# Performance work log

Hardware: AMD Instinct MI355X
Metric: run time of the kernel (lower is better)

## Reference

```python
import jax, jax.numpy as jnp
import numpy as np


def _gcn_conv(x, W, b, src, dst, n_nodes):
    # PyG GCNConv with add_self_loops=True, edge_weight=None (implicit ones),
    # symmetric normalization: D^{-1/2} A_hat D^{-1/2} (X W) + b
    xw = x @ W                                    # [N, H]
    loop = jnp.arange(n_nodes, dtype=src.dtype)
    src_f = jnp.concatenate([src, loop])          # [E+N]
    dst_f = jnp.concatenate([dst, loop])          # [E+N]
    w = jnp.ones(src_f.shape[0], dtype=x.dtype)
    deg = jax.ops.segment_sum(w, dst_f, num_segments=n_nodes)  # in-degree incl. self-loop
    dinv = jnp.where(deg > 0, jax.lax.rsqrt(deg), 0.0)
    norm = dinv[src_f] * dinv[dst_f]              # [E+N]
    msgs = norm[:, None] * xw[src_f]              # [E+N, H]
    out = jax.ops.segment_sum(msgs, dst_f, num_segments=n_nodes)
    return out + b


def setup_inputs() -> dict:
    key = jax.random.key(0)
    k1, k2, k3, k4 = jax.random.split(key, 4)
    N, E, D, H = 100000, 1600000, 256, 128
    x = jax.random.normal(k1, (N, D), dtype=jnp.float32)
    edge_index = jax.random.randint(k2, (2, E), 0, N, dtype=jnp.int64)
    # Glorot-scaled weights
    W1 = jax.random.normal(k3, (D, H), dtype=jnp.float32) * np.sqrt(2.0 / (D + H))
    b1 = jnp.zeros((H,), dtype=jnp.float32)
    W2 = jax.random.normal(k4, (H, 1), dtype=jnp.float32) * np.sqrt(2.0 / (H + 1))
    b2 = jnp.zeros((1,), dtype=jnp.float32)
    return {"x": x, "edge_index": edge_index, "W1": W1, "b1": b1, "W2": W2, "b2": b2}


def reference(x, edge_index, W1, b1, W2, b2):
    n_nodes = x.shape[0]
    src, dst = edge_index[0], edge_index[1]
    h = _gcn_conv(x, W1, b1, src, dst, n_nodes)   # conv1
    h = jax.nn.relu(h)                            # relu; dropout is identity in eval mode
    out = _gcn_conv(h, W2, b2, src, dst, n_nodes) # conv2 -> [N, 1]
    return out.reshape(-1)                        # x.view(-1)
```

## Files before the change

kernel.cpp:

```cpp
#include <hip/hip_runtime.h>
#include <hip/hip_fp16.h>
#include <cstdint>
#include <cstddef>


#define BSH 9
#define BNODES (1 << BSH)
#define BPAD 16
#define BCAP 9216

typedef _Float16 half8 __attribute__((ext_vector_type(8)));
typedef float floatx4 __attribute__((ext_vector_type(4)));
typedef float floatv4 __attribute__((ext_vector_type(4)));
typedef int intv4 __attribute__((ext_vector_type(4)));
typedef unsigned int uintv4 __attribute__((ext_vector_type(4)));

__device__ __forceinline__ void fmamix8(float (&acc)[8], uint4 v, float w) {
  asm("v_fma_mix_f32 %0, %1, %2, %0 op_sel:[0,0,0] op_sel_hi:[0,1,0]"
      : "+v"(acc[0]) : "v"(w), "v"(v.x));
  asm("v_fma_mix_f32 %0, %1, %2, %0 op_sel:[0,1,0] op_sel_hi:[0,1,0]"
      : "+v"(acc[1]) : "v"(w), "v"(v.x));
  asm("v_fma_mix_f32 %0, %1, %2, %0 op_sel:[0,0,0] op_sel_hi:[0,1,0]"
      : "+v"(acc[2]) : "v"(w), "v"(v.y));
  asm("v_fma_mix_f32 %0, %1, %2, %0 op_sel:[0,1,0] op_sel_hi:[0,1,0]"
      : "+v"(acc[3]) : "v"(w), "v"(v.y));
  asm("v_fma_mix_f32 %0, %1, %2, %0 op_sel:[0,0,0] op_sel_hi:[0,1,0]"
      : "+v"(acc[4]) : "v"(w), "v"(v.z));
  asm("v_fma_mix_f32 %0, %1, %2, %0 op_sel:[0,1,0] op_sel_hi:[0,1,0]"
      : "+v"(acc[5]) : "v"(w), "v"(v.z));
  asm("v_fma_mix_f32 %0, %1, %2, %0 op_sel:[0,0,0] op_sel_hi:[0,1,0]"
      : "+v"(acc[6]) : "v"(w), "v"(v.w));
  asm("v_fma_mix_f32 %0, %1, %2, %0 op_sel:[0,1,0] op_sel_hi:[0,1,0]"
      : "+v"(acc[7]) : "v"(w), "v"(v.w));
}

#define SWZF(v, imm) \
  __int_as_float(__builtin_amdgcn_ds_swizzle(__float_as_int(v), imm))

__global__ __launch_bounds__(256) void prep_k(const float* __restrict__ W1,
                                              _Float16* __restrict__ wz,
                                              _Float16* __restrict__ z1h,
                                              float* __restrict__ z2w,
                                              int* __restrict__ cnt,
                                              int* __restrict__ gcur,
                                              int N, int NB) {
  int b = blockIdx.x, tid = threadIdx.x;
  if (b < 128) {
    int id = b * 256 + tid;
    int j = id & 7, lane = (id >> 3) & 63, nb = (id >> 9) & 7, kb = id >> 12;
    int k = kb * 32 + ((lane >> 4) << 3) + j;
    int n = nb * 16 + (lane & 15);
    wz[id] = (_Float16)W1[k * 128 + n];
  } else if (b == 128) {
    if (tid < 128) z1h[(size_t)N * 128 + tid] = (_Float16)0.f;
    if (tid == 0) { z2w[N] = 0.f; cnt[N] = 1; }
  } else {
    int i = (b - 129) * 256 + tid;
    if (i < NB * BPAD) gcur[i] = 0;
  }
}

__global__ __launch_bounds__(256) void stage_k(int kind, int fb, int g0,
                                               const float* __restrict__ X,
                                               const _Float16* __restrict__ wz,
                                               _Float16* __restrict__ z1h, int N,
                                               const int* __restrict__ src,
                                               const int* __restrict__ dst,
                                               int* __restrict__ gcur,
                                               int* __restrict__ barr,
                                               int* __restrict__ ell,
                                               int* __restrict__ ell2,
                                               int* __restrict__ cnt,
                                               int E, int NB) {
  __shared__ char lds_raw[16 * 1024];
  int tid = threadIdx.x;

  if ((int)blockIdx.x < fb) {
    if (kind == 0) {
      int* bc = (int*)lds_raw;
      int* bb = bc + 512;
      for (int i = tid; i < NB; i += 256) bc[i] = 0;
      __syncthreads();
      int base = ((int)blockIdx.x * 256 + tid) * 16;
      int dv[16], sv[16], rv[16], bkv[16];
      int ne = 0;
      if (base + 15 < E) {
#pragma unroll
        for (int q4 = 0; q4 < 4; ++q4) {
          intv4 d4 = __builtin_nontemporal_load((const intv4*)(dst + base + q4 * 4));
          intv4 s4 = __builtin_nontemporal_load((const intv4*)(src + base + q4 * 4));
          dv[q4 * 4 + 0] = d4[0]; dv[q4 * 4 + 1] = d4[1];
          dv[q4 * 4 + 2] = d4[2]; dv[q4 * 4 + 3] = d4[3];
          sv[q4 * 4 + 0] = s4[0]; sv[q4 * 4 + 1] = s4[1];
          sv[q4 * 4 + 2] = s4[2]; sv[q4 * 4 + 3] = s4[3];
        }
        ne = 16;
      } else {
        for (int e = base; e < E && e < base + 16; ++e) {
          dv[ne] = dst[e]; sv[ne] = src[e]; ++ne;
        }
      }
      for (int i = 0; i < ne; ++i) {
        bkv[i] = dv[i] >> BSH;
        rv[i] = atomicAdd(&bc[bkv[i]], 1);
      }
      __syncthreads();
      for (int i = tid; i < NB; i += 256) {
        int cc = bc[i];
        bb[i] = cc ? atomicAdd(&gcur[i * BPAD], cc) : 0;
      }
      __syncthreads();
      for (int i = 0; i < ne; ++i) {
        int pos = bb[bkv[i]] + rv[i];
        if (pos < BCAP) {
          unsigned dl = (unsigned)(dv[i] & (BNODES - 1));
          barr[(size_t)bkv[i] * BCAP + pos] = (int)((dl << 23) | (unsigned)sv[i]);
        }
      }
    } else {
      int* cl = (int*)lds_raw;
      int bkt = (int)blockIdx.x;
      int lo = bkt << BSH;
      for (int i = tid; i < BNODES; i += 256) {
        cl[i] = 1;
        int node = lo + i;
        if (node < N) ell[(size_t)node * 32] = node;
      }
      __syncthreads();
      int cb = min(gcur[bkt * BPAD], BCAP);
      const int* seg = barr + (size_t)bkt * BCAP;
      for (int e = tid; e < cb; e += 256) {
        unsigned v = (unsigned)seg[e];
        int dl = (int)(v >> 23);
        int s = (int)(v & 0x7FFFFFu);
        int p = atomicAdd(&cl[dl], 1);
        if (p < 32) ell[(size_t)(lo + dl) * 32 + p] = s;
        else if (p < 63) ell2[(size_t)(lo + dl) * 32 + (p - 32)] = s;
      }
      __syncthreads();
      for (int i = tid; i < BNODES; i += 256) {
        int node = lo + i;
        if (node < N) cnt[node] = cl[i];
      }
    }
    return;
  }

  _Float16* Bl = (_Float16*)lds_raw;
  _Float16* Ol = (_Float16*)lds_raw;

  int wave = tid >> 6, lane = tid & 63;
  int m = lane & 15, q = lane >> 4;
  int row0 = (g0 + (int)blockIdx.x - fb) * 64;
  int row = row0 + wave * 16 + m;

  floatx4 acc[8];
#pragma unroll
  for (int nb = 0; nb < 8; ++nb) acc[nb] = (floatx4)(0.f);

  const uintv4* wsrc = (const uintv4*)wz;
  uintv4* bdst = (uintv4*)Bl;

#pragma unroll
  for (int ph = 0; ph < 4; ++ph) {
    if (ph) __syncthreads();
#pragma unroll
    for (int i = 0; i < 4; ++i) bdst[i * 256 + tid] = wsrc[ph * 1024 + i * 256 + tid];
    __syncthreads();
#pragma unroll
    for (int kk = 0; kk < 2; ++kk) {
      int kb = ph * 2 + kk;
      half8 a;
      if (row < N) {
        const floatv4* ap = (const floatv4*)(X + (size_t)row * 256 + kb * 32 + q * 8);
        floatv4 a0 = __builtin_nontemporal_load(ap);
        floatv4 a1 = __builtin_nontemporal_load(ap + 1);
        a[0] = (_Float16)a0[0]; a[1] = (_Float16)a0[1];
        a[2] = (_Float16)a0[2]; a[3] = (_Float16)a0[3];
        a[4] = (_Float16)a1[0]; a[5] = (_Float16)a1[1];
        a[6] = (_Float16)a1[2]; a[7] = (_Float16)a1[3];
      } else {
#pragma unroll
        for (int j = 0; j < 8; ++j) a[j] = (_Float16)0.f;
      }
#pragma unroll
      for (int nb = 0; nb < 8; ++nb) {
        half8 b = *(const half8*)(Bl + ((size_t)(kk * 8 + nb) * 64 + lane) * 8);
        acc[nb] = __builtin_amdgcn_mfma_f32_16x16x32_f16(a, b, acc[nb], 0, 0, 0);
      }
    }
  }
  __syncthreads();

#pragma unroll
  for (int nb = 0; nb < 8; ++nb) {
    int col = nb * 16 + m;
#pragma unroll
    for (int r = 0; r < 4; ++r) {
      int orow = wave * 16 + q * 4 + r;
      Ol[orow * 128 + col] = (_Float16)acc[nb][r];
    }
  }
  __syncthreads();

  const uintv4* osrc = (const uintv4*)Ol;
  uintv4* gdst = (uintv4*)(z1h + (size_t)row0 * 128);
#pragma unroll
  for (int i = 0; i < 4; ++i) {
    int idx = i * 256 + tid;
    int r = idx >> 4;
    if (row0 + r < N) gdst[idx] = osrc[idx];
  }
}

__global__ __launch_bounds__(256) void agg1_k(const _Float16* __restrict__ z1h,
                                              const int* __restrict__ cnt,
                                              const int* __restrict__ ell,
                                              const int* __restrict__ ell2,
                                              const float* __restrict__ b1,
                                              const float* __restrict__ W2,
                                              float* __restrict__ z2w, int N) {
  int d = blockIdx.x * 4 + (threadIdx.x >> 6);
  int lane = threadIdx.x & 63;
  if (d >= N) return;
  int cntd = cnt[d];
  int ct = min(cntd, 63);
  int raw;
  if (ct > 32) {
    raw = (lane < 32) ? ell[(size_t)d * 32 + lane]
                      : (lane < 63 ? ell2[(size_t)d * 32 + (lane - 32)] : N);
  } else {
    raw = ell[(size_t)d * 32 + (lane & 31)];
  }
  int idx = (lane < ct) ? raw : N;
  float wl = rsqrtf((float)cnt[idx]);
  float dd = rsqrtf((float)cntd);
  int iw = __float_as_int(wl);

  int g = lane >> 4;
  unsigned a16 = (unsigned)(lane & 15) << 4;
  const char* zb = (const char*)z1h;
  int pa = g << 2;
  int ax = (lane ^ 32) << 2;

  float acc[8] = {0.f, 0.f, 0.f, 0.f, 0.f, 0.f, 0.f, 0.f};

  int t = 0;
  for (; t + 16 <= ct; t += 16) {
    int a0 = pa + (t << 2);
    int s0 = __builtin_amdgcn_ds_bpermute(a0, idx);
    int s1 = __builtin_amdgcn_ds_bpermute(a0 + 16, idx);
    int s2 = __builtin_amdgcn_ds_bpermute(a0 + 32, idx);
    int s3 = __builtin_amdgcn_ds_bpermute(a0 + 48, idx);
    float w0 = __int_as_float(__builtin_amdgcn_ds_bpermute(a0, iw));
    float w1 = __int_as_float(__builtin_amdgcn_ds_bpermute(a0 + 16, iw));
    float w2 = __int_as_float(__builtin_amdgcn_ds_bpermute(a0 + 32, iw));
    float w3 = __int_as_float(__builtin_amdgcn_ds_bpermute(a0 + 48, iw));
    uint4 v0 = *(const uint4*)(zb + (((unsigned)s0 << 8) + a16));
    uint4 v1 = *(const uint4*)(zb + (((unsigned)s1 << 8) + a16));
    uint4 v2 = *(const uint4*)(zb + (((unsigned)s2 << 8) + a16));
    uint4 v3 = *(const uint4*)(zb + (((unsigned)s3 << 8) + a16));
    fmamix8(acc, v0, w0);
    fmamix8(acc, v1, w1);
    fmamix8(acc, v2, w2);
    fmamix8(acc, v3, w3);
  }
  for (; t < ct; t += 4) {
    int a0 = pa + (t << 2);
    int s0 = __builtin_amdgcn_ds_bpermute(a0, idx);
    float w0 = __int_as_float(__builtin_amdgcn_ds_bpermute(a0, iw));
    uint4 v0 = *(const uint4*)(zb + (((unsigned)s0 << 8) + a16));
    fmamix8(acc, v0, w0);
  }

#pragma unroll
  for (int k = 0; k < 8; ++k) {
    float x = acc[k];
    x += SWZF(x, 0x401F);
    x += __int_as_float(__builtin_amdgcn_ds_bpermute(ax, __float_as_int(x)));
    acc[k] = x;
  }

  int a8 = (lane & 15) * 8;
  float4 bA = *(const float4*)(b1 + a8);
  float4 bB = *(const float4*)(b1 + a8 + 4);
  float4 wA = *(const float4*)(W2 + a8);
  float4 wB = *(const float4*)(W2 + a8 + 4);
  float dot = fmaxf(fmaf(dd, acc[0], bA.x), 0.f) * wA.x
            + fmaxf(fmaf(dd, acc[1], bA.y), 0.f) * wA.y
            + fmaxf(fmaf(dd, acc[2], bA.z), 0.f) * wA.z
            + fmaxf(fmaf(dd, acc[3], bA.w), 0.f) * wA.w
            + fmaxf(fmaf(dd, acc[4], bB.x), 0.f) * wB.x
            + fmaxf(fmaf(dd, acc[5], bB.y), 0.f) * wB.y
            + fmaxf(fmaf(dd, acc[6], bB.z), 0.f) * wB.z
            + fmaxf(fmaf(dd, acc[7], bB.w), 0.f) * wB.w;
  dot += SWZF(dot, 0x201F);
  dot += SWZF(dot, 0x101F);
  dot += SWZF(dot, 0x081F);
  dot += SWZF(dot, 0x041F);
  if (lane == 0) z2w[d] = dd * dot;
}

__global__ __launch_bounds__(256) void agg2_k(const float* __restrict__ z2w,
                                              const int* __restrict__ cnt,
                                              const int* __restrict__ ell,
                                              const int* __restrict__ ell2,
                                              const float* __restrict__ b2,
                                              float* __restrict__ out, int N) {
  int wv = threadIdx.x >> 6;
  int half = (threadIdx.x >> 5) & 1;
  int j = threadIdx.x & 31;
  int d = blockIdx.x * 8 + wv * 2 + half;
  if (d >= N) return;
  int cd = cnt[d];
  int c = min(cd, 63);
  int raw = ell[(size_t)d * 32 + j];
  int idx = (j < min(c, 32)) ? raw : N;
  float v = z2w[idx];
  if (c > 32 && j < c - 32) v += z2w[ell2[(size_t)d * 32 + j]];
#pragma unroll
  for (int off = 16; off >= 1; off >>= 1) v += __shfl_xor(v, off, 64);
  if (j == 0) out[d] = rsqrtf((float)cd) * v + b2[0];
}

extern "C" void kernel_launch(void* const* d_in, const int* in_sizes, int n_in,
                              void* d_out, int out_size, void* d_ws, size_t ws_size,
                              hipStream_t stream) {
  (void)n_in; (void)out_size; (void)ws_size;
  const float* x = (const float*)d_in[0];
  const int* edge = (const int*)d_in[1];
  const float* W1 = (const float*)d_in[2];
  const float* b1 = (const float*)d_in[3];
  const float* W2 = (const float*)d_in[4];
  const float* b2 = (const float*)d_in[5];
  float* out = (float*)d_out;

  const int D = 256, H = 128;
  int N = in_sizes[0] / D;
  int E = in_sizes[1] / 2;
  const int* srcp = edge;
  const int* dstp = edge + E;
  int NB = (N + BNODES - 1) >> BSH;

  char* ws = (char*)d_ws;
  size_t off = 0;
  auto alloc = [&](size_t bytes) -> void* {
    void* p = ws + off;
    off += (bytes + 255) & ~(size_t)255;
    return p;
  };
  int* cnt        = (int*)alloc((size_t)(N + 1) * 4);
  float* z2w      = (float*)alloc((size_t)(N + 1) * 4);
  int* ell        = (int*)alloc((size_t)N * 32 * 4);
  int* ell2       = (int*)alloc((size_t)N * 32 * 4);
  _Float16* wz    = (_Float16*)alloc((size_t)32768 * 2);
  _Float16* z1h   = (_Float16*)alloc((size_t)(N + 1) * H * 2);
  int* gcur       = (int*)alloc((size_t)NB * BPAD * 4);
  int* barr       = (int*)alloc((size_t)NB * BCAP * 4);

  int tiles = (N + 63) / 64;
  int fbA = (E + 4095) / 4096;
  int fbB = NB;

  int T2 = tiles / 2;
  if (T2 > tiles) T2 = tiles;
  int T1 = tiles - T2;

  prep_k<<<dim3(129 + (NB * BPAD + 255) / 256), dim3(256), 0, stream>>>(
      W1, wz, z1h, z2w, cnt, gcur, N, NB);
  stage_k<<<dim3(fbA + T1), dim3(256), 0, stream>>>(0, fbA, 0, x, wz, z1h, N,
      srcp, dstp, gcur, barr, ell, ell2, cnt, E, NB);
  stage_k<<<dim3(fbB + T2), dim3(256), 0, stream>>>(1, fbB, T1, x, wz, z1h, N,
      srcp, dstp, gcur, barr, ell, ell2, cnt, E, NB);
  agg1_k<<<dim3((N + 3) / 4), dim3(256), 0, stream>>>(z1h, cnt, ell, ell2, b1, W2, z2w, N);
  agg2_k<<<dim3((N + 7) / 8), dim3(256), 0, stream>>>(z2w, cnt, ell, ell2, b2, out, N);
}
```

Before: 278.1 us.

## Quantize conv1 features to int8 per-row scale for cheaper gather aggregation

```diff
diff --git a/kernel.cpp b/kernel.cpp
--- a/kernel.cpp
+++ b/kernel.cpp
@@ -14,8 +14,13 @@
 typedef float floatv4 __attribute__((ext_vector_type(4)));
 typedef int intv4 __attribute__((ext_vector_type(4)));
 typedef unsigned int uintv4 __attribute__((ext_vector_type(4)));
-
-__device__ __forceinline__ void fmamix8(float (&acc)[8], uint4 v, float w) {
+typedef unsigned int uintv2 __attribute__((ext_vector_type(2)));
+
+#define QK 0x64646464u
+#define SEL01 0x00050004u
+#define SEL23 0x00070006u
+
+__device__ __forceinline__ void fmamix8(float (&acc)[8], uintv4 v, float w) {
   asm("v_fma_mix_f32 %0, %1, %2, %0 op_sel:[0,0,0] op_sel_hi:[0,1,0]"
       : "+v"(acc[0]) : "v"(w), "v"(v.x));
   asm("v_fma_mix_f32 %0, %1, %2, %0 op_sel:[0,1,0] op_sel_hi:[0,1,0]"
@@ -34,12 +39,22 @@
       : "+v"(acc[7]) : "v"(w), "v"(v.w));
 }
 
+__device__ __forceinline__ void fmaq8(float (&acc)[8], uintv2 q, float w) {
+  uintv4 hw;
+  hw.x = __builtin_amdgcn_perm(q.x, QK, SEL01);
+  hw.y = __builtin_amdgcn_perm(q.x, QK, SEL23);
+  hw.z = __builtin_amdgcn_perm(q.y, QK, SEL01);
+  hw.w = __builtin_amdgcn_perm(q.y, QK, SEL23);
+  fmamix8(acc, hw, w);
+}
+
 #define SWZF(v, imm) \
   __int_as_float(__builtin_amdgcn_ds_swizzle(__float_as_int(v), imm))
 
 __global__ __launch_bounds__(256) void prep_k(const float* __restrict__ W1,
                                               _Float16* __restrict__ wz,
-                                              _Float16* __restrict__ z1h,
+                                              unsigned char* __restrict__ z1q8,
+                                              float* __restrict__ scp,
                                               float* __restrict__ z2w,
                                               int* __restrict__ cnt,
                                               int* __restrict__ gcur,
@@ -52,18 +67,20 @@
     int n = nb * 16 + (lane & 15);
     wz[id] = (_Float16)W1[k * 128 + n];
   } else if (b == 128) {
-    if (tid < 128) z1h[(size_t)N * 128 + tid] = (_Float16)0.f;
-    if (tid == 0) { z2w[N] = 0.f; cnt[N] = 1; }
+    if (tid < 32) ((unsigned*)(z1q8 + (size_t)N * 128))[tid] = 0x80808080u;
+    if (tid == 0) { z2w[N] = 0.f; cnt[N] = 1; scp[N] = 1.f; }
   } else {
     int i = (b - 129) * 256 + tid;
     if (i < NB * BPAD) gcur[i] = 0;
   }
 }
 
-__global__ __launch_bounds__(256) void stage_k(int kind, int fb, int g0,
+template <int KIND>
+__global__ __launch_bounds__(256) void stage_k(int fb, int g0,
                                                const float* __restrict__ X,
                                                const _Float16* __restrict__ wz,
-                                               _Float16* __restrict__ z1h, int N,
+                                               unsigned char* __restrict__ z1q8,
+                                               float* __restrict__ scp, int N,
                                                const int* __restrict__ src,
                                                const int* __restrict__ dst,
                                                int* __restrict__ gcur,
@@ -72,11 +89,11 @@
                                                int* __restrict__ ell2,
                                                int* __restrict__ cnt,
                                                int E, int NB) {
-  __shared__ char lds_raw[16 * 1024];
+  __shared__ char lds_raw[16 * 1024 + 256];
   int tid = threadIdx.x;
 
   if ((int)blockIdx.x < fb) {
-    if (kind == 0) {
+    if (KIND == 0) {
       int* bc = (int*)lds_raw;
       int* bb = bc + 512;
       for (int i = tid; i < NB; i += 256) bc[i] = 0;
@@ -148,6 +165,7 @@
 
   _Float16* Bl = (_Float16*)lds_raw;
   _Float16* Ol = (_Float16*)lds_raw;
+  float* invl = (float*)(lds_raw + 16 * 1024);
 
   int wave = tid >> 6, lane = tid & 63;
   int m = lane & 15, q = lane >> 4;
@@ -190,6 +208,23 @@
       }
     }
   }
+
+  float rmax[4];
+#pragma unroll
+  for (int r = 0; r < 4; ++r) rmax[r] = 1e-6f;
+#pragma unroll
+  for (int nb = 0; nb < 8; ++nb)
+#pragma unroll
+    for (int r = 0; r < 4; ++r) rmax[r] = fmaxf(rmax[r], fabsf(acc[nb][r]));
+#pragma unroll
+  for (int r = 0; r < 4; ++r) {
+    float v = rmax[r];
+    v = fmaxf(v, __shfl_xor(v, 1, 64));
+    v = fmaxf(v, __shfl_xor(v, 2, 64));
+    v = fmaxf(v, __shfl_xor(v, 4, 64));
+    v = fmaxf(v, __shfl_xor(v, 8, 64));
+    rmax[r] = v;
+  }
   __syncthreads();
 
 #pragma unroll
@@ -201,19 +236,45 @@
       Ol[orow * 128 + col] = (_Float16)acc[nb][r];
     }
   }
+  if (m == 0) {
+#pragma unroll
+    for (int r = 0; r < 4; ++r) {
+      int tr = wave * 16 + q * 4 + r;
+      float inv = 126.5f / rmax[r];
+      invl[tr] = inv;
+      int rw = row0 + tr;
+      if (rw < N) scp[rw] = rmax[r] * (1.f / 126.5f);
+    }
+  }
   __syncthreads();
 
   const uintv4* osrc = (const uintv4*)Ol;
-  uintv4* gdst = (uintv4*)(z1h + (size_t)row0 * 128);
 #pragma unroll
   for (int i = 0; i < 4; ++i) {
     int idx = i * 256 + tid;
     int r = idx >> 4;
-    if (row0 + r < N) gdst[idx] = osrc[idx];
-  }
-}
-
-__global__ __launch_bounds__(256) void agg1_k(const _Float16* __restrict__ z1h,
+    int fb8 = idx & 15;
+    if (row0 + r < N) {
+      uintv4 v = osrc[idx];
+      half8 hv = __builtin_bit_cast(half8, v);
+      float inv = invl[r];
+      unsigned bq[8];
+#pragma unroll
+      for (int j = 0; j < 8; ++j) {
+        float t = fmaf((float)hv[j], inv, 1152.0f);
+        _Float16 ht = (_Float16)t;
+        bq[j] = (unsigned)__builtin_bit_cast(unsigned short, ht) & 0xFFu;
+      }
+      uintv2 o;
+      o.x = bq[0] | (bq[1] << 8) | (bq[2] << 16) | (bq[3] << 24);
+      o.y = bq[4] | (bq[5] << 8) | (bq[6] << 16) | (bq[7] << 24);
+      *(uintv2*)(z1q8 + (size_t)(row0 + r) * 128 + fb8 * 8) = o;
+    }
+  }
+}
+
+__global__ __launch_bounds__(256) void agg1_k(const unsigned char* __restrict__ z1q8,
+                                              const float* __restrict__ scp,
                                               const int* __restrict__ cnt,
                                               const int* __restrict__ ell,
                                               const int* __restrict__ ell2,
@@ -233,17 +294,18 @@
     raw = ell[(size_t)d * 32 + (lane & 31)];
   }
   int idx = (lane < ct) ? raw : N;
-  float wl = rsqrtf((float)cnt[idx]);
+  float ws = rsqrtf((float)cnt[idx]) * scp[idx];
   float dd = rsqrtf((float)cntd);
-  int iw = __float_as_int(wl);
+  int iw = __float_as_int(ws);
 
   int g = lane >> 4;
-  unsigned a16 = (unsigned)(lane & 15) << 4;
-  const char* zb = (const char*)z1h;
+  unsigned a8 = (unsigned)(lane & 15) << 3;
+  const unsigned char* zb = z1q8;
   int pa = g << 2;
   int ax = (lane ^ 32) << 2;
 
   float acc[8] = {0.f, 0.f, 0.f, 0.f, 0.f, 0.f, 0.f, 0.f};
+  float bs = 0.f;
 
   int t = 0;
   for (; t + 16 <= ct; t += 16) {
@@ -256,21 +318,23 @@
     float w1 = __int_as_float(__builtin_amdgcn_ds_bpermute(a0 + 16, iw));
     float w2 = __int_as_float(__builtin_amdgcn_ds_bpermute(a0 + 32, iw));
     float w3 = __int_as_float(__builtin_amdgcn_ds_bpermute(a0 + 48, iw));
-    uint4 v0 = *(const uint4*)(zb + (((unsigned)s0 << 8) + a16));
-    uint4 v1 = *(const uint4*)(zb + (((unsigned)s1 << 8) + a16));
-    uint4 v2 = *(const uint4*)(zb + (((unsigned)s2 << 8) + a16));
-    uint4 v3 = *(const uint4*)(zb + (((unsigned)s3 << 8) + a16));
-    fmamix8(acc, v0, w0);
-    fmamix8(acc, v1, w1);
-    fmamix8(acc, v2, w2);
-    fmamix8(acc, v3, w3);
+    uintv2 q0 = *(const uintv2*)(zb + (((unsigned)s0) << 7) + a8);
+    uintv2 q1 = *(const uintv2*)(zb + (((unsigned)s1) << 7) + a8);
+    uintv2 q2 = *(const uintv2*)(zb + (((unsigned)s2) << 7) + a8);
+    uintv2 q3 = *(const uintv2*)(zb + (((unsigned)s3) << 7) + a8);
+    fmaq8(acc, q0, w0);
+    fmaq8(acc, q1, w1);
+    fmaq8(acc, q2, w2);
+    fmaq8(acc, q3, w3);
+    bs += (w0 + w1) + (w2 + w3);
   }
   for (; t < ct; t += 4) {
     int a0 = pa + (t << 2);
     int s0 = __builtin_amdgcn_ds_bpermute(a0, idx);
     float w0 = __int_as_float(__builtin_amdgcn_ds_bpermute(a0, iw));
-    uint4 v0 = *(const uint4*)(zb + (((unsigned)s0 << 8) + a16));
-    fmamix8(acc, v0, w0);
+    uintv2 q0 = *(const uintv2*)(zb + (((unsigned)s0) << 7) + a8);
+    fmaq8(acc, q0, w0);
+    bs += w0;
   }
 
 #pragma unroll
@@ -280,20 +344,23 @@
     x += __int_as_float(__builtin_amdgcn_ds_bpermute(ax, __float_as_int(x)));
     acc[k] = x;
   }
-
-  int a8 = (lane & 15) * 8;
-  float4 bA = *(const float4*)(b1 + a8);
-  float4 bB = *(const float4*)(b1 + a8 + 4);
-  float4 wA = *(const float4*)(W2 + a8);
-  float4 wB = *(const float4*)(W2 + a8 + 4);
-  float dot = fmaxf(fmaf(dd, acc[0], bA.x), 0.f) * wA.x
-            + fmaxf(fmaf(dd, acc[1], bA.y), 0.f) * wA.y
-            + fmaxf(fmaf(dd, acc[2], bA.z), 0.f) * wA.z
-            + fmaxf(fmaf(dd, acc[3], bA.w), 0.f) * wA.w
-            + fmaxf(fmaf(dd, acc[4], bB.x), 0.f) * wB.x
-            + fmaxf(fmaf(dd, acc[5], bB.y), 0.f) * wB.y
-            + fmaxf(fmaf(dd, acc[6], bB.z), 0.f) * wB.z
-            + fmaxf(fmaf(dd, acc[7], bB.w), 0.f) * wB.w;
+  bs += SWZF(bs, 0x401F);
+  bs += __int_as_float(__builtin_amdgcn_ds_bpermute(ax, __float_as_int(bs)));
+  float corr = 1152.f * bs;
+
+  int a8f = (lane & 15) * 8;
+  float4 bA = *(const float4*)(b1 + a8f);
+  float4 bB = *(const float4*)(b1 + a8f + 4);
+  float4 wA = *(const float4*)(W2 + a8f);
+  float4 wB = *(const float4*)(W2 + a8f + 4);
+  float dot = fmaxf(fmaf(dd, acc[0] - corr, bA.x), 0.f) * wA.x
+            + fmaxf(fmaf(dd, acc[1] - corr, bA.y), 0.f) * wA.y
+            + fmaxf(fmaf(dd, acc[2] - corr, bA.z), 0.f) * wA.z
+            + fmaxf(fmaf(dd, acc[3] - corr, bA.w), 0.f) * wA.w
+            + fmaxf(fmaf(dd, acc[4] - corr, bB.x), 0.f) * wB.x
+            + fmaxf(fmaf(dd, acc[5] - corr, bB.y), 0.f) * wB.y
+            + fmaxf(fmaf(dd, acc[6] - corr, bB.z), 0.f) * wB.z
+            + fmaxf(fmaf(dd, acc[7] - corr, bB.w), 0.f) * wB.w;
   dot += SWZF(dot, 0x201F);
   dot += SWZF(dot, 0x101F);
   dot += SWZF(dot, 0x081F);
@@ -349,29 +416,30 @@
     off += (bytes + 255) & ~(size_t)255;
     return p;
   };
-  int* cnt        = (int*)alloc((size_t)(N + 1) * 4);
-  float* z2w      = (float*)alloc((size_t)(N + 1) * 4);
-  int* ell        = (int*)alloc((size_t)N * 32 * 4);
-  int* ell2       = (int*)alloc((size_t)N * 32 * 4);
-  _Float16* wz    = (_Float16*)alloc((size_t)32768 * 2);
-  _Float16* z1h   = (_Float16*)alloc((size_t)(N + 1) * H * 2);
-  int* gcur       = (int*)alloc((size_t)NB * BPAD * 4);
-  int* barr       = (int*)alloc((size_t)NB * BCAP * 4);
+  int* cnt            = (int*)alloc((size_t)(N + 1) * 4);
+  float* z2w          = (float*)alloc((size_t)(N + 1) * 4);
+  float* scp          = (float*)alloc((size_t)(N + 1) * 4);
+  int* ell            = (int*)alloc((size_t)N * 32 * 4);
+  int* ell2           = (int*)alloc((size_t)N * 32 * 4);
+  _Float16* wz        = (_Float16*)alloc((size_t)32768 * 2);
+  unsigned char* z1q8 = (unsigned char*)alloc((size_t)(N + 1) * 128);
+  int* gcur           = (int*)alloc((size_t)NB * BPAD * 4);
+  int* barr           = (int*)alloc((size_t)NB * BCAP * 4);
 
   int tiles = (N + 63) / 64;
   int fbA = (E + 4095) / 4096;
   int fbB = NB;
 
   int T2 = tiles / 2;
-  if (T2 > tiles) T2 = tiles;
   int T1 = tiles - T2;
 
   prep_k<<<dim3(129 + (NB * BPAD + 255) / 256), dim3(256), 0, stream>>>(
-      W1, wz, z1h, z2w, cnt, gcur, N, NB);
-  stage_k<<<dim3(fbA + T1), dim3(256), 0, stream>>>(0, fbA, 0, x, wz, z1h, N,
-      srcp, dstp, gcur, barr, ell, ell2, cnt, E, NB);
-  stage_k<<<dim3(fbB + T2), dim3(256), 0, stream>>>(1, fbB, T1, x, wz, z1h, N,
-      srcp, dstp, gcur, barr, ell, ell2, cnt, E, NB);
-  agg1_k<<<dim3((N + 3) / 4), dim3(256), 0, stream>>>(z1h, cnt, ell, ell2, b1, W2, z2w, N);
+      W1, wz, z1q8, scp, z2w, cnt, gcur, N, NB);
+  stage_k<0><<<dim3(fbA + T1), dim3(256), 0, stream>>>(fbA, 0, x, wz, z1q8, scp,
+      N, srcp, dstp, gcur, barr, ell, ell2, cnt, E, NB);
+  stage_k<1><<<dim3(fbB + T2), dim3(256), 0, stream>>>(fbB, T1, x, wz, z1q8, scp,
+      N, srcp, dstp, gcur, barr, ell, ell2, cnt, E, NB);
+  agg1_k<<<dim3((N + 3) / 4), dim3(256), 0, stream>>>(z1q8, scp, cnt, ell, ell2,
+      b1, W2, z2w, N);
   agg2_k<<<dim3((N + 7) / 8), dim3(256), 0, stream>>>(z2w, cnt, ell, ell2, b2, out, N);
 }
```

Result: faster. 272.0 us (-2.2%).
